# Performance work log

Hardware: AMD Instinct MI355X
Metric: run time of the kernel (lower is better)

Reference implementation:

```python
import jax, jax.numpy as jnp
import numpy as np

NUM_CLUSTERS = 64  # real clusters (ghost clusters excluded from residuals)
EPS = 1e-12        # F.normalize eps


def setup_inputs() -> dict:
    key = jax.random.key(0)
    k1, k2, k3 = jax.random.split(key, 3)
    x = jax.random.normal(k1, (8, 128, 32, 32), dtype=jnp.float32)
    # 1x1 conv weight [K+G, C] (kernel spatial dims squeezed), no bias (vladv2=False)
    conv_w = jax.random.normal(k2, (68, 128), dtype=jnp.float32) * 0.05
    centroids = jax.random.uniform(k3, (68, 128), dtype=jnp.float32)
    return {"x": x, "conv_w": conv_w, "centroids": centroids}


def reference(x, conv_w, centroids):
    # x: [N,C,H,W]; conv_w: [K+G,C]; centroids: [K+G,C]
    # descriptor-wise L2 normalization over channel dim (normalize_input=True)
    nrm = jnp.sqrt(jnp.sum(x * x, axis=1, keepdims=True))
    xn = x / jnp.maximum(nrm, EPS)
    # 1x1 conv -> soft assignment logits over K+G clusters, softmax over cluster dim
    logits = jnp.einsum('nchw,kc->nkhw', xn, conv_w)
    soft_assign = jax.nn.softmax(logits, axis=1)            # [N,K+G,H,W]
    # fused per-cluster residual: (x - c_k) * a_k, only real clusters
    resid = (xn[:, None, :, :, :] -
             centroids[:NUM_CLUSTERS][None, :, :, None, None])  # [N,K,C,H,W]
    store_residual = resid * soft_assign[:, :NUM_CLUSTERS, None, :, :]
    return store_residual, soft_assign
```

## Files before the change

kernel.cpp:

```cpp
#include <hip/hip_runtime.h>

#define PIMG 1024
#define CCH  128
#define KG   68
#define KR   64
#define T1   32

typedef float f4v __attribute__((ext_vector_type(4)));

__global__ __launch_bounds__(256) void nv_assign_kernel(
    const float* __restrict__ x,
    const float* __restrict__ conv_w,
    float* __restrict__ sa_out,
    float* __restrict__ rnorm_ws)
{
    __shared__ float xs[CCH * T1];
    __shared__ float lg[KG * T1];
    __shared__ float red[8 * T1];
    __shared__ float rn_l[T1];
    __shared__ float mx_l[T1];
    __shared__ float is_l[T1];

    const int t   = threadIdx.x;
    const int gp0 = blockIdx.x * T1;
    const int n   = gp0 >> 10;
    const int p0  = gp0 & 1023;

    const float* xb = x + (size_t)n * (CCH * PIMG) + p0;
    for (int i = t; i < CCH * T1; i += 256)
        xs[i] = xb[(i >> 5) * PIMG + (i & 31)];
    __syncthreads();

    {
        int pix = t & 31, q = t >> 5;
        float s = 0.f;
        #pragma unroll
        for (int c = q * 16; c < q * 16 + 16; ++c) {
            float v = xs[c * T1 + pix];
            s += v * v;
        }
        red[q * T1 + pix] = s;
    }
    __syncthreads();
    if (t < T1) {
        float s = 0.f;
        #pragma unroll
        for (int q = 0; q < 8; ++q) s += red[q * T1 + t];
        float r = 1.0f / fmaxf(sqrtf(s), 1e-12f);
        rn_l[t] = r;
        rnorm_ws[gp0 + t] = r;
    }
    __syncthreads();

    for (int task = t; task < (KG / 2) * (T1 / 4); task += 256) {
        int g  = task & 7;
        int k0 = (task >> 3) << 1;
        const float* w0 = conv_w + k0 * CCH;
        const float* w1 = w0 + CCH;
        f4v a0 = {0.f, 0.f, 0.f, 0.f}, a1 = {0.f, 0.f, 0.f, 0.f};
        #pragma unroll 8
        for (int c = 0; c < CCH; ++c) {
            f4v xv = *(const f4v*)(xs + c * T1 + g * 4);
            float wv0 = w0[c], wv1 = w1[c];
            a0 += xv * wv0;
            a1 += xv * wv1;
        }
        f4v r4 = *(const f4v*)(rn_l + g * 4);
        *(f4v*)(lg + k0 * T1 + g * 4)       = a0 * r4;
        *(f4v*)(lg + (k0 + 1) * T1 + g * 4) = a1 * r4;
    }
    __syncthreads();

    {
        int pix = t & 31, q = t >> 5;
        float m = -1e30f;
        for (int k = q; k < KG; k += 8) m = fmaxf(m, lg[k * T1 + pix]);
        red[q * T1 + pix] = m;
    }
    __syncthreads();
    if (t < T1) {
        float m = red[t];
        #pragma unroll
        for (int q = 1; q < 8; ++q) m = fmaxf(m, red[q * T1 + t]);
        mx_l[t] = m;
    }
    __syncthreads();
    {
        int pix = t & 31, q = t >> 5;
        float m = mx_l[pix], s = 0.f;
        for (int k = q; k < KG; k += 8) {
            float e = expf(lg[k * T1 + pix] - m);
            lg[k * T1 + pix] = e;
            s += e;
        }
        red[q * T1 + pix] = s;
    }
    __syncthreads();
    if (t < T1) {
        float s = 0.f;
        #pragma unroll
        for (int q = 0; q < 8; ++q) s += red[q * T1 + t];
        is_l[t] = 1.0f / s;
    }
    __syncthreads();

    for (int i = t; i < KG * T1; i += 256) {
        int k = i >> 5, pix = i & 31;
        sa_out[((size_t)n * KG + k) * PIMG + p0 + pix] = lg[i] * is_l[pix];
    }
}

__global__ __launch_bounds__(256) void nv_resid_kernel(
    const float* __restrict__ x,
    const float* __restrict__ centroids,
    const float* __restrict__ sa,
    const float* __restrict__ rnorm,
    float* __restrict__ out)
{
    const int b  = blockIdx.x;
    const int n  = b >> 8;
    const int k  = (b >> 2) & 63;
    const int c0 = (b & 3) << 5;
    const int t  = threadIdx.x;

    const f4v rn4 = ((const f4v*)(rnorm + (size_t)n * PIMG))[t];
    const f4v a4  = ((const f4v*)(sa + ((size_t)n * KG + k) * PIMG))[t];
    const f4v ra  = rn4 * a4;

    const float* cw = centroids + k * CCH + c0;
    const float* xb = x + (size_t)n * (CCH * PIMG) + (size_t)c0 * PIMG;
    float* ob = out + (((size_t)n * KR + k) * CCH + c0) * PIMG;

    #pragma unroll 8
    for (int c = 0; c < 32; ++c) {
        f4v xv = ((const f4v*)(xb + c * PIMG))[t];
        float ce = cw[c];
        f4v o = xv * ra - ce * a4;
        ((f4v*)(ob + c * PIMG))[t] = o;
    }
}

extern "C" void kernel_launch(void* const* d_in, const int* in_sizes, int n_in,
                              void* d_out, int out_size, void* d_ws, size_t ws_size,
                              hipStream_t stream) {
    const float* x         = (const float*)d_in[0];
    const float* conv_w    = (const float*)d_in[1];
    const float* centroids = (const float*)d_in[2];

    const int N = in_sizes[0] / (CCH * PIMG);

    float* out    = (float*)d_out;
    float* sa_out = out + (size_t)N * KR * CCH * PIMG;
    float* rnorm  = (float*)d_ws;

    nv_assign_kernel<<<N * (PIMG / T1), 256, 0, stream>>>(x, conv_w, sa_out, rnorm);
    nv_resid_kernel<<<N * KR * 4, 256, 0, stream>>>(x, centroids, sa_out, rnorm, out);
}
```

Before: 63.13 us.

## Restructure residual kernel to loop over clusters with channels held in registers

The residual kernel now gives each block 4 channels and 32 clusters instead of 1 cluster and 32 channels. Normalized x values are kept in registers and reused across clusters, and soft-assign rows are streamed from memory. This cuts redundant reads of x in exchange for more soft-assign reads. The grid shrinks from 2048 blocks to 512, which may reduce the number of waves in flight for a store-bound kernel on a large GPU.

```diff
diff --git a/kernel.cpp b/kernel.cpp
--- a/kernel.cpp
+++ b/kernel.cpp
@@ -118,25 +118,34 @@
     float* __restrict__ out)
 {
     const int b  = blockIdx.x;
-    const int n  = b >> 8;
-    const int k  = (b >> 2) & 63;
-    const int c0 = (b & 3) << 5;
+    const int cs = b & 31;
+    const int kh = (b >> 5) & 1;
+    const int n  = b >> 6;
+    const int c0 = cs * 4;
+    const int k0 = kh * 32;
     const int t  = threadIdx.x;
 
     const f4v rn4 = ((const f4v*)(rnorm + (size_t)n * PIMG))[t];
-    const f4v a4  = ((const f4v*)(sa + ((size_t)n * KG + k) * PIMG))[t];
-    const f4v ra  = rn4 * a4;
 
-    const float* cw = centroids + k * CCH + c0;
     const float* xb = x + (size_t)n * (CCH * PIMG) + (size_t)c0 * PIMG;
-    float* ob = out + (((size_t)n * KR + k) * CCH + c0) * PIMG;
+    f4v xn[4];
+    #pragma unroll
+    for (int c = 0; c < 4; ++c)
+        xn[c] = ((const f4v*)(xb + c * PIMG))[t] * rn4;
 
-    #pragma unroll 8
-    for (int c = 0; c < 32; ++c) {
-        f4v xv = ((const f4v*)(xb + c * PIMG))[t];
-        float ce = cw[c];
-        f4v o = xv * ra - ce * a4;
-        ((f4v*)(ob + c * PIMG))[t] = o;
+    const float* sab = sa + (size_t)n * KG * PIMG;
+    const float* cwb = centroids + c0;
+    float* ob = out + ((size_t)n * KR * CCH + (size_t)c0) * PIMG;
+
+    #pragma unroll 4
+    for (int k = k0; k < k0 + 32; ++k) {
+        f4v a4 = ((const f4v*)(sab + (size_t)k * PIMG))[t];
+        #pragma unroll
+        for (int c = 0; c < 4; ++c) {
+            float ce = cwb[k * CCH + c];
+            f4v o = (xn[c] - ce) * a4;
+            ((f4v*)(ob + ((size_t)k * CCH + c) * PIMG))[t] = o;
+        }
     }
 }
 
@@ -154,5 +163,5 @@
     float* rnorm  = (float*)d_ws;
 
     nv_assign_kernel<<<N * (PIMG / T1), 256, 0, stream>>>(x, conv_w, sa_out, rnorm);
-    nv_resid_kernel<<<N * KR * 4, 256, 0, stream>>>(x, centroids, sa_out, rnorm, out);
+    nv_resid_kernel<<<N * 2 * 32, 256, 0, stream>>>(x, centroids, sa_out, rnorm, out);
 }
```

Measured after the change: 63.51 us. Within noise of the previous version (+0.6%).

## Keep per-pixel channel vector in registers and split clusters across waves

Applied to the files above, without the earlier changes.

The assign kernel now covers 64 pixels per block. Each of the four waves loads the full 128-channel vector for its lane's pixel into registers, computes the norm locally, and handles a strided quarter of the clusters with wave-uniform weight loads. This removes the shared-memory x tile and the norm reduction barrier. The cost is heavy register use (128 floats per thread), redundant x loads across the four waves, and half as many blocks. The residual kernel, which dominates output bandwidth, is unchanged.

```diff
diff --git a/kernel.cpp b/kernel.cpp
--- a/kernel.cpp
+++ b/kernel.cpp
@@ -4,7 +4,7 @@
 #define CCH  128
 #define KG   68
 #define KR   64
-#define T1   32
+#define T1   64
 
 typedef float f4v __attribute__((ext_vector_type(4)));
 
@@ -14,99 +14,79 @@
     float* __restrict__ sa_out,
     float* __restrict__ rnorm_ws)
 {
-    __shared__ float xs[CCH * T1];
-    __shared__ float lg[KG * T1];
-    __shared__ float red[8 * T1];
-    __shared__ float rn_l[T1];
+    __shared__ float lg[KG][T1 + 2];
+    __shared__ float red[4][T1];
     __shared__ float mx_l[T1];
     __shared__ float is_l[T1];
 
-    const int t   = threadIdx.x;
-    const int gp0 = blockIdx.x * T1;
-    const int n   = gp0 >> 10;
-    const int p0  = gp0 & 1023;
+    const int t    = threadIdx.x;
+    const int lane = t & 63;
+    const int wv   = __builtin_amdgcn_readfirstlane(t >> 6);
+    const int gp0  = blockIdx.x * T1;
+    const int n    = gp0 >> 10;
+    const int p0   = gp0 & 1023;
 
-    const float* xb = x + (size_t)n * (CCH * PIMG) + p0;
-    for (int i = t; i < CCH * T1; i += 256)
-        xs[i] = xb[(i >> 5) * PIMG + (i & 31)];
-    __syncthreads();
+    const float* xp = x + (size_t)n * (CCH * PIMG) + p0 + lane;
+    float xr[CCH];
+    #pragma unroll
+    for (int c = 0; c < CCH; ++c) xr[c] = xp[c * PIMG];
 
-    {
-        int pix = t & 31, q = t >> 5;
-        float s = 0.f;
+    float s0 = 0.f, s1 = 0.f, s2 = 0.f, s3 = 0.f;
+    #pragma unroll
+    for (int c = 0; c < CCH; c += 4) {
+        s0 += xr[c + 0] * xr[c + 0];
+        s1 += xr[c + 1] * xr[c + 1];
+        s2 += xr[c + 2] * xr[c + 2];
+        s3 += xr[c + 3] * xr[c + 3];
+    }
+    const float rn = 1.0f / fmaxf(sqrtf((s0 + s1) + (s2 + s3)), 1e-12f);
+    if (t < T1) rnorm_ws[gp0 + t] = rn;
+
+    #pragma unroll
+    for (int c = 0; c < CCH; ++c) xr[c] *= rn;
+
+    #pragma unroll 2
+    for (int k = wv; k < KG; k += 4) {
+        const float* wr = conv_w + k * CCH;
+        float a0 = 0.f, a1 = 0.f, a2 = 0.f, a3 = 0.f;
         #pragma unroll
-        for (int c = q * 16; c < q * 16 + 16; ++c) {
-            float v = xs[c * T1 + pix];
-            s += v * v;
+        for (int c = 0; c < CCH; c += 4) {
+            a0 += xr[c + 0] * wr[c + 0];
+            a1 += xr[c + 1] * wr[c + 1];
+            a2 += xr[c + 2] * wr[c + 2];
+            a3 += xr[c + 3] * wr[c + 3];
         }
-        red[q * T1 + pix] = s;
-    }
-    __syncthreads();
-    if (t < T1) {
-        float s = 0.f;
-        #pragma unroll
-        for (int q = 0; q < 8; ++q) s += red[q * T1 + t];
-        float r = 1.0f / fmaxf(sqrtf(s), 1e-12f);
-        rn_l[t] = r;
-        rnorm_ws[gp0 + t] = r;
-    }
-    __syncthreads();
-
-    for (int task = t; task < (KG / 2) * (T1 / 4); task += 256) {
-        int g  = task & 7;
-        int k0 = (task >> 3) << 1;
-        const float* w0 = conv_w + k0 * CCH;
-        const float* w1 = w0 + CCH;
-        f4v a0 = {0.f, 0.f, 0.f, 0.f}, a1 = {0.f, 0.f, 0.f, 0.f};
-        #pragma unroll 8
-        for (int c = 0; c < CCH; ++c) {
-            f4v xv = *(const f4v*)(xs + c * T1 + g * 4);
-            float wv0 = w0[c], wv1 = w1[c];
-            a0 += xv * wv0;
-            a1 += xv * wv1;
-        }
-        f4v r4 = *(const f4v*)(rn_l + g * 4);
-        *(f4v*)(lg + k0 * T1 + g * 4)       = a0 * r4;
-        *(f4v*)(lg + (k0 + 1) * T1 + g * 4) = a1 * r4;
+        lg[k][lane] = (a0 + a1) + (a2 + a3);
     }
     __syncthreads();
 
     {
-        int pix = t & 31, q = t >> 5;
         float m = -1e30f;
-        for (int k = q; k < KG; k += 8) m = fmaxf(m, lg[k * T1 + pix]);
-        red[q * T1 + pix] = m;
+        for (int k = wv; k < KG; k += 4) m = fmaxf(m, lg[k][lane]);
+        red[wv][lane] = m;
     }
     __syncthreads();
-    if (t < T1) {
-        float m = red[t];
-        #pragma unroll
-        for (int q = 1; q < 8; ++q) m = fmaxf(m, red[q * T1 + t]);
-        mx_l[t] = m;
+    if (t < T1)
+        mx_l[t] = fmaxf(fmaxf(red[0][t], red[1][t]),
+                        fmaxf(red[2][t], red[3][t]));
+    __syncthreads();
+    {
+        float m = mx_l[lane], s = 0.f;
+        for (int k = wv; k < KG; k += 4) {
+            float e = expf(lg[k][lane] - m);
+            lg[k][lane] = e;
+            s += e;
+        }
+        red[wv][lane] = s;
     }
     __syncthreads();
-    {
-        int pix = t & 31, q = t >> 5;
-        float m = mx_l[pix], s = 0.f;
-        for (int k = q; k < KG; k += 8) {
-            float e = expf(lg[k * T1 + pix] - m);
-            lg[k * T1 + pix] = e;
-            s += e;
-        }
-        red[q * T1 + pix] = s;
-    }
-    __syncthreads();
-    if (t < T1) {
-        float s = 0.f;
-        #pragma unroll
-        for (int q = 0; q < 8; ++q) s += red[q * T1 + t];
-        is_l[t] = 1.0f / s;
-    }
+    if (t < T1)
+        is_l[t] = 1.0f / (red[0][t] + red[1][t] + red[2][t] + red[3][t]);
     __syncthreads();
 
     for (int i = t; i < KG * T1; i += 256) {
-        int k = i >> 5, pix = i & 31;
-        sa_out[((size_t)n * KG + k) * PIMG + p0 + pix] = lg[i] * is_l[pix];
+        int k = i >> 6, pix = i & 63;
+        sa_out[((size_t)n * KG + k) * PIMG + p0 + pix] = lg[k][pix] * is_l[pix];
     }
 }
 
```

Result: slower. 113.6 us (+80.0%).
